# Optimization experiments

Hardware: AMD Instinct MI355X
Metric: run time of the kernel (lower is better)

The kernel has to match this reference:

```python
import jax, jax.numpy as jnp
import numpy as np

HD, NH, DH, NL = 768, 16, 48, 3
EPS = 1e-5


def _ln(x, p):
    g, b = p[0], p[1]
    mu = x.mean(-1, keepdims=True)
    var = ((x - mu) ** 2).mean(-1, keepdims=True)
    return (x - mu) * jax.lax.rsqrt(var + EPS) * g + b


def _init_mlp(x, w1, b1, ln1, w2, b2, ln2):
    h = jax.nn.relu(_ln(x @ w1.T + b1, ln1))
    return jnp.tanh(_ln(h @ w2.T + b2, ln2))


def setup_inputs() -> dict:
    B, S, V = 64, 32, 32000
    key = jax.random.key(0)
    ks = iter(jax.random.split(key, 64))
    rn = lambda shape, s=0.02: jax.random.normal(next(ks), shape, jnp.float32) * s
    lnp = lambda d: jnp.stack([jnp.ones(d, jnp.float32), jnp.zeros(d, jnp.float32)])
    emb = rn((V, 512)).at[0].set(0.0)  # padding_idx=0
    inp = {
        'word_ids': jax.random.randint(next(ks), (B, S), 0, V, jnp.int32),
        'cnn_feat': jax.random.normal(next(ks), (B, HD), jnp.float32),
        'attn_feat': jax.random.normal(next(ks), (B, 2048, 7, 7), jnp.float32),
        'emb': emb,
        'attn_f_w': rn((HD, 2048)), 'attn_f_b': rn((HD,)),
        'attn_qkv_w': rn((3, HD, HD)), 'attn_qkv_b': rn((3, HD)),
        'attn_o_w': rn((HD, HD)), 'attn_o_b': rn((HD,)), 'attn_ln': lnp(HD),
        'fus_w1': rn((HD, 512 + HD)), 'fus_b1': rn((HD,)), 'fus_ln1': lnp(HD),
        'fus_w2': rn((HD, HD)), 'fus_b2': rn((HD,)), 'fus_ln2': lnp(HD),
        'lstm_wih': rn((NL, 4 * HD, HD)), 'lstm_whh': rn((NL, 4 * HD, HD)),
        'lstm_bih': rn((NL, 4 * HD)), 'lstm_bhh': rn((NL, 4 * HD)),
        'hinit_w1': rn((2 * HD, HD)), 'hinit_b1': rn((2 * HD,)), 'hinit_ln1': lnp(2 * HD),
        'hinit_w2': rn((HD, 2 * HD)), 'hinit_b2': rn((HD,)), 'hinit_ln2': lnp(HD),
        'cinit_w1': rn((2 * HD, HD)), 'cinit_b1': rn((2 * HD,)), 'cinit_ln1': lnp(2 * HD),
        'cinit_w2': rn((HD, 2 * HD)), 'cinit_b2': rn((HD,)), 'cinit_ln2': lnp(HD),
        'out_w1': rn((2 * HD, HD)), 'out_b1': rn((2 * HD,)), 'out_ln1': lnp(2 * HD),
        'out_w2': rn((HD, 2 * HD)), 'out_b2': rn((HD,)), 'out_ln2': lnp(HD),
        'out_w3': rn((V, HD)), 'out_b3': rn((V,)),
    }
    return inp


def _forward(word_ids, cnn_feat, attn_feat, emb,
             attn_f_w, attn_f_b, attn_qkv_w, attn_qkv_b, attn_o_w, attn_o_b, attn_ln,
             fus_w1, fus_b1, fus_ln1, fus_w2, fus_b2, fus_ln2,
             lstm_wih, lstm_whh, lstm_bih, lstm_bhh,
             hinit_w1, hinit_b1, hinit_ln1, hinit_w2, hinit_b2, hinit_ln2,
             cinit_w1, cinit_b1, cinit_ln1, cinit_w2, cinit_b2, cinit_ln2,
             out_w1, out_b1, out_ln1, out_w2, out_b2, out_ln2, out_w3, out_b3):
    B, S = word_ids.shape
    # feature projection + K/V are timestep-independent -> hoist out of the loop
    feat = attn_feat.reshape(B, 2048, 49).transpose(0, 2, 1)          # (B,49,2048)
    fp = feat @ attn_f_w.T + attn_f_b                                  # (B,49,HD)
    Wq, Wk, Wv = attn_qkv_w[0], attn_qkv_w[1], attn_qkv_w[2]
    bq, bk, bv = attn_qkv_b[0], attn_qkv_b[1], attn_qkv_b[2]
    K = (fp @ Wk.T + bk).reshape(B, 49, NH, DH).transpose(0, 2, 1, 3)  # (B,NH,49,DH)
    V = (fp @ Wv.T + bv).reshape(B, 49, NH, DH).transpose(0, 2, 1, 3)

    h0 = _init_mlp(cnn_feat, hinit_w1, hinit_b1, hinit_ln1, hinit_w2, hinit_b2, hinit_ln2)
    c0 = _init_mlp(cnn_feat, cinit_w1, cinit_b1, cinit_ln1, cinit_w2, cinit_b2, cinit_ln2)
    h = jnp.tile(h0[None], (NL, 1, 1))                                 # (NL,B,HD)
    c = jnp.tile(c0[None], (NL, 1, 1))

    embeds = emb[word_ids]                                             # (B,S,512)
    scale = np.float32(1.0 / np.sqrt(DH))

    def step(carry, e_t):
        h, c = carry
        q = (h[-1] @ Wq.T + bq).reshape(B, NH, DH)
        scores = jnp.einsum('bhd,bhkd->bhk', q, K) * scale
        w = jax.nn.softmax(scores, axis=-1)
        ctx = jnp.einsum('bhk,bhkd->bhd', w, V).reshape(B, HD)
        ctx = _ln(ctx @ attn_o_w.T + attn_o_b, attn_ln)
        x = jnp.concatenate([e_t, ctx], axis=1)                        # (B,512+HD)
        x = jax.nn.relu(_ln(x @ fus_w1.T + fus_b1, fus_ln1))
        x = jax.nn.relu(_ln(x @ fus_w2.T + fus_b2, fus_ln2))
        inp = x
        hs, cs = [], []
        for l in range(NL):
            g = inp @ lstm_wih[l].T + lstm_bih[l] + h[l] @ lstm_whh[l].T + lstm_bhh[l]
            i, f, gg, o = jnp.split(g, 4, axis=-1)                     # torch gate order
            cn = jax.nn.sigmoid(f) * c[l] + jax.nn.sigmoid(i) * jnp.tanh(gg)
            hn = jax.nn.sigmoid(o) * jnp.tanh(cn)
            hs.append(hn); cs.append(cn); inp = hn
        h = jnp.stack(hs); c = jnp.stack(cs)
        y = jax.nn.relu(_ln(inp @ out_w1.T + out_b1, out_ln1))
        y = jax.nn.relu(_ln(y @ out_w2.T + out_b2, out_ln2))
        logits = y @ out_w3.T + out_b3                                 # (B,V)
        return (h, c), logits

    (hf, cf), ys = jax.lax.scan(step, (h, c), embeds.transpose(1, 0, 2))
    return ys.transpose(1, 0, 2), hf, cf


def reference(word_ids, cnn_feat, attn_feat, emb,
              attn_f_w, attn_f_b, attn_qkv_w, attn_qkv_b, attn_o_w, attn_o_b, attn_ln,
              fus_w1, fus_b1, fus_ln1, fus_w2, fus_b2, fus_ln2,
              lstm_wih, lstm_whh, lstm_bih, lstm_bhh,
              hinit_w1, hinit_b1, hinit_ln1, hinit_w2, hinit_b2, hinit_ln2,
              cinit_w1, cinit_b1, cinit_ln1, cinit_w2, cinit_b2, cinit_ln2,
              out_w1, out_b1, out_ln1, out_w2, out_b2, out_ln2, out_w3, out_b3):
    return _forward(word_ids, cnn_feat, attn_feat, emb,
                    attn_f_w, attn_f_b, attn_qkv_w, attn_qkv_b, attn_o_w, attn_o_b, attn_ln,
                    fus_w1, fus_b1, fus_ln1, fus_w2, fus_b2, fus_ln2,
                    lstm_wih, lstm_whh, lstm_bih, lstm_bhh,
                    hinit_w1, hinit_b1, hinit_ln1, hinit_w2, hinit_b2, hinit_ln2,
                    cinit_w1, cinit_b1, cinit_ln1, cinit_w2, cinit_b2, cinit_ln2,
                    out_w1, out_b1, out_ln1, out_w2, out_b2, out_ln2, out_w3, out_b3)
```

## Files before the change

kernel.cpp:

```cpp
#include <hip/hip_runtime.h>
#include <hip/hip_bf16.h>

enum { B_ = 64, S_ = 32, V_ = 32000, HDIM = 768, NHEAD = 16, DHEAD = 48, NLAY = 3 };
#define LN_EPS 1e-5f

typedef __bf16 bf16_t;
typedef __bf16 bf8 __attribute__((ext_vector_type(8)));
typedef __bf16 bf4v __attribute__((ext_vector_type(4)));
typedef float f4 __attribute__((ext_vector_type(4)));

__device__ __forceinline__ float sigm(float x) { return 1.f / (1.f + expf(-x)); }

__device__ __forceinline__ f4 mfma16x16x32(bf8 a, bf8 b, f4 c) {
    return __builtin_amdgcn_mfma_f32_16x16x32_bf16(a, b, c, 0, 0, 0);
}

__global__ __launch_bounds__(256) void cast_bf16_4(const float4* __restrict__ x,
                                                   bf4v* __restrict__ y, int n4) {
    int i = blockIdx.x * 256 + threadIdx.x;
    int st = gridDim.x * 256;
    for (; i < n4; i += st) {
        float4 v = x[i];
        bf4v o;
        o.x = (__bf16)v.x; o.y = (__bf16)v.y; o.z = (__bf16)v.z; o.w = (__bf16)v.w;
        y[i] = o;
    }
}

template <int OUTBF, int REMAP>
__global__ __launch_bounds__(256) void gemm_mf(const bf16_t* __restrict__ A, int lda,
                                               const bf16_t* __restrict__ W, int ldw,
                                               const float* __restrict__ bias,
                                               void* __restrict__ Cv, int ldc, int K) {
    const int lane = threadIdx.x & 63, wv = threadIdx.x >> 6;
    const int r = lane & 15, kg = lane >> 4;
    const int m0 = blockIdx.y * 64 + wv * 16;
    const int n0 = blockIdx.x * 64;
    const bf16_t* Ar = A + (size_t)(m0 + r) * lda + kg * 8;
    const bf16_t* W0 = W + (size_t)(n0 + r) * ldw + kg * 8;
    f4 acc[4] = {};
#pragma unroll 2
    for (int k0 = 0; k0 < K; k0 += 32) {
        bf8 a = *(const bf8*)(Ar + k0);
#pragma unroll
        for (int j = 0; j < 4; ++j) {
            bf8 b = *(const bf8*)(W0 + (size_t)j * 16 * ldw + k0);
            acc[j] = mfma16x16x32(a, b, acc[j]);
        }
    }
#pragma unroll
    for (int j = 0; j < 4; ++j) {
        int n = n0 + j * 16 + r;
        float bz = bias[n];
#pragma unroll
        for (int i = 0; i < 4; ++i) {
            int m = m0 + kg * 4 + i;
            float v = acc[j][i] + bz;
            if (REMAP) {
                int tt = m >> 6, bb = m & 63;
                ((float*)Cv)[((size_t)bb * S_ + tt) * V_ + n] = v;
            } else if (OUTBF) {
                ((bf16_t*)Cv)[(size_t)m * ldc + n] = (__bf16)v;
            } else {
                ((float*)Cv)[(size_t)m * ldc + n] = v;
            }
        }
    }
}

__global__ __launch_bounds__(256) void gemm_lstm(const bf16_t* __restrict__ X,
                                                 const bf16_t* __restrict__ Wih,
                                                 const bf16_t* __restrict__ H,
                                                 const bf16_t* __restrict__ Whh,
                                                 const float* __restrict__ b1,
                                                 const float* __restrict__ b2,
                                                 float* __restrict__ G) {
    const int lane = threadIdx.x & 63, wv = threadIdx.x >> 6;
    const int r = lane & 15, kg = lane >> 4;
    const int m0 = wv * 16;
    const int n0 = blockIdx.x * 64;
    const bf16_t* Xr = X + (size_t)(m0 + r) * HDIM + kg * 8;
    const bf16_t* Hr = H + (size_t)(m0 + r) * HDIM + kg * 8;
    const bf16_t* Wi = Wih + (size_t)(n0 + r) * HDIM + kg * 8;
    const bf16_t* Wh = Whh + (size_t)(n0 + r) * HDIM + kg * 8;
    f4 acc[4] = {};
#pragma unroll 2
    for (int k0 = 0; k0 < HDIM; k0 += 32) {
        bf8 ax = *(const bf8*)(Xr + k0);
        bf8 ah = *(const bf8*)(Hr + k0);
#pragma unroll
        for (int j = 0; j < 4; ++j) {
            acc[j] = mfma16x16x32(ax, *(const bf8*)(Wi + (size_t)j * 16 * HDIM + k0), acc[j]);
            acc[j] = mfma16x16x32(ah, *(const bf8*)(Wh + (size_t)j * 16 * HDIM + k0), acc[j]);
        }
    }
#pragma unroll
    for (int j = 0; j < 4; ++j) {
        int n = n0 + j * 16 + r;
        float bz = b1[n] + b2[n];
#pragma unroll
        for (int i = 0; i < 4; ++i) {
            int m = m0 + kg * 4 + i;
            G[(size_t)m * (4 * HDIM) + n] = acc[j][i] + bz;
        }
    }
}

__global__ __launch_bounds__(256) void gemm_fus1(const bf16_t* __restrict__ embB,
                                                 const bf16_t* __restrict__ ctxB, int t,
                                                 const bf16_t* __restrict__ W,
                                                 const float* __restrict__ bias,
                                                 float* __restrict__ C) {
    const int lane = threadIdx.x & 63, wv = threadIdx.x >> 6;
    const int r = lane & 15, kg = lane >> 4;
    const int m0 = wv * 16;
    const int n0 = blockIdx.x * 64;
    const int mr = m0 + r;
    const bf16_t* W0 = W + (size_t)(n0 + r) * 1280 + kg * 8;
    const bf16_t* eRow = embB + ((size_t)mr * S_ + t) * 512 + kg * 8;
    const bf16_t* cRow = ctxB + (size_t)mr * HDIM + kg * 8;
    f4 acc[4] = {};
#pragma unroll 2
    for (int k0 = 0; k0 < 1280; k0 += 32) {
        bf8 a = (k0 < 512) ? *(const bf8*)(eRow + k0) : *(const bf8*)(cRow + (k0 - 512));
#pragma unroll
        for (int j = 0; j < 4; ++j) {
            bf8 b = *(const bf8*)(W0 + (size_t)j * 16 * 1280 + k0);
            acc[j] = mfma16x16x32(a, b, acc[j]);
        }
    }
#pragma unroll
    for (int j = 0; j < 4; ++j) {
        int n = n0 + j * 16 + r;
        float bz = bias[n];
#pragma unroll
        for (int i = 0; i < 4; ++i) {
            int m = m0 + kg * 4 + i;
            C[(size_t)m * HDIM + n] = acc[j][i] + bz;
        }
    }
}

__global__ __launch_bounds__(256) void transpose_feat(const float* __restrict__ af,
                                                      bf16_t* __restrict__ feat) {
    __shared__ float t[32][33];
    int b = blockIdx.z;
    int c0 = blockIdx.x * 32;
    int p0 = blockIdx.y * 32;
    int tx = threadIdx.x, ty = threadIdx.y;
    const float* src = af + (size_t)b * 2048 * 49;
    for (int i = ty; i < 32; i += 8) {
        int c = c0 + i, p = p0 + tx;
        t[i][tx] = (p < 49) ? src[(size_t)c * 49 + p] : 0.f;
    }
    __syncthreads();
    bf16_t* dst = feat + (size_t)b * 49 * 2048;
    for (int i = ty; i < 32; i += 8) {
        int p = p0 + i, c = c0 + tx;
        if (p < 49) dst[(size_t)p * 2048 + c] = (__bf16)t[tx][i];
    }
}

__global__ void gather_emb(const int* __restrict__ ids, const float* __restrict__ emb,
                           bf16_t* __restrict__ out) {
    int r = blockIdx.x;
    int w = ids[r];
    const float* e = emb + (size_t)w * 512;
    bf16_t* o = out + (size_t)r * 512;
    for (int i = threadIdx.x; i < 512; i += 256) o[i] = (__bf16)e[i];
}

__global__ __launch_bounds__(256) void ln_act(const float* __restrict__ X,
                                              const float* __restrict__ lnp,
                                              float* __restrict__ Y,
                                              bf16_t* __restrict__ Yb, int N, int act) {
    int r = blockIdx.x;
    const float* x = X + (size_t)r * N;
    float* y = Y + (size_t)r * N;
    bf16_t* yb = Yb ? (Yb + (size_t)r * N) : nullptr;
    float s1 = 0.f, s2 = 0.f;
    for (int i = threadIdx.x; i < N; i += 256) {
        float v = x[i];
        s1 += v;
        s2 += v * v;
    }
#pragma unroll
    for (int off = 32; off > 0; off >>= 1) {
        s1 += __shfl_down(s1, off, 64);
        s2 += __shfl_down(s2, off, 64);
    }
    __shared__ float a1[4], a2[4];
    __shared__ float mu_s, rs_s;
    int lane = threadIdx.x & 63, wid = threadIdx.x >> 6;
    if (lane == 0) { a1[wid] = s1; a2[wid] = s2; }
    __syncthreads();
    if (threadIdx.x == 0) {
        float S1 = a1[0] + a1[1] + a1[2] + a1[3];
        float S2 = a2[0] + a2[1] + a2[2] + a2[3];
        float mu = S1 / N;
        float var = S2 / N - mu * mu;
        mu_s = mu;
        rs_s = rsqrtf(var + LN_EPS);
    }
    __syncthreads();
    float mu = mu_s, rs = rs_s;
    for (int i = threadIdx.x; i < N; i += 256) {
        float v = (x[i] - mu) * rs * lnp[i] + lnp[N + i];
        if (act == 1) v = fmaxf(v, 0.f);
        else if (act == 2) v = tanhf(v);
        y[i] = v;
        if (yb) yb[i] = (__bf16)v;
    }
}

__global__ __launch_bounds__(64) void attn_ctx(const float* __restrict__ q,
                                               const float* __restrict__ Kf,
                                               const float* __restrict__ Vf,
                                               bf16_t* __restrict__ ctx) {
    int b = blockIdx.x, h = blockIdx.y;
    int t = threadIdx.x;
    __shared__ float qs[48];
    __shared__ float w[49];
    if (t < 48) qs[t] = q[(size_t)b * HDIM + h * DHEAD + t];
    __syncthreads();
    if (t < 49) {
        const float* kr = Kf + (size_t)(b * 49 + t) * HDIM + h * DHEAD;
        float s = 0.f;
#pragma unroll
        for (int d = 0; d < 48; ++d) s += qs[d] * kr[d];
        w[t] = s * 0.14433756729740643f;
    }
    __syncthreads();
    if (t == 0) {
        float mx = w[0];
        for (int p = 1; p < 49; ++p) mx = fmaxf(mx, w[p]);
        float sum = 0.f;
        for (int p = 0; p < 49; ++p) {
            float e = expf(w[p] - mx);
            w[p] = e;
            sum += e;
        }
        float inv = 1.f / sum;
        for (int p = 0; p < 49; ++p) w[p] *= inv;
    }
    __syncthreads();
    if (t < 48) {
        float acc = 0.f;
        for (int p = 0; p < 49; ++p) acc += w[p] * Vf[(size_t)(b * 49 + p) * HDIM + h * DHEAD + t];
        ctx[(size_t)b * HDIM + h * DHEAD + t] = (__bf16)acc;
    }
}

__global__ void lstm_cell(const float* __restrict__ g, float* __restrict__ c,
                          float* __restrict__ h, bf16_t* __restrict__ hb,
                          bf16_t* __restrict__ Hcb, int t) {
    int idx = blockIdx.x * 256 + threadIdx.x;
    if (idx >= B_ * HDIM) return;
    int b = idx / HDIM, j = idx - b * HDIM;
    const float* gr = g + (size_t)b * 4 * HDIM;
    float iv = sigm(gr[j]);
    float fv = sigm(gr[HDIM + j]);
    float gv = tanhf(gr[2 * HDIM + j]);
    float ov = sigm(gr[3 * HDIM + j]);
    float cn = fv * c[idx] + iv * gv;
    float hn = ov * tanhf(cn);
    c[idx] = cn;
    h[idx] = hn;
    hb[idx] = (__bf16)hn;
    if (Hcb) Hcb[((size_t)t * B_ + b) * HDIM + j] = (__bf16)hn;
}

__global__ void tile_state(const float* __restrict__ h0, const float* __restrict__ c0,
                           float* __restrict__ h, float* __restrict__ c,
                           bf16_t* __restrict__ hb) {
    int idx = blockIdx.x * 256 + threadIdx.x;
    if (idx >= B_ * HDIM) return;
    float hv = h0[idx], cv = c0[idx];
#pragma unroll
    for (int l = 0; l < NLAY; ++l) {
        h[(size_t)l * B_ * HDIM + idx] = hv;
        c[(size_t)l * B_ * HDIM + idx] = cv;
        hb[(size_t)l * B_ * HDIM + idx] = (__bf16)hv;
    }
}

extern "C" void kernel_launch(void* const* d_in, const int* in_sizes, int n_in,
                              void* d_out, int out_size, void* d_ws, size_t ws_size,
                              hipStream_t stream) {
    const int* word_ids  = (const int*)d_in[0];
    const float* cnn     = (const float*)d_in[1];
    const float* attn_f  = (const float*)d_in[2];
    const float* emb     = (const float*)d_in[3];
    const float* af_w    = (const float*)d_in[4];
    const float* af_b    = (const float*)d_in[5];
    const float* qkv_w   = (const float*)d_in[6];
    const float* qkv_b   = (const float*)d_in[7];
    const float* o_w     = (const float*)d_in[8];
    const float* o_b     = (const float*)d_in[9];
    const float* attn_ln = (const float*)d_in[10];
    const float* fus_w1  = (const float*)d_in[11];
    const float* fus_b1  = (const float*)d_in[12];
    const float* fus_ln1 = (const float*)d_in[13];
    const float* fus_w2  = (const float*)d_in[14];
    const float* fus_b2  = (const float*)d_in[15];
    const float* fus_ln2 = (const float*)d_in[16];
    const float* wih     = (const float*)d_in[17];
    const float* whh     = (const float*)d_in[18];
    const float* bih     = (const float*)d_in[19];
    const float* bhh     = (const float*)d_in[20];
    const float* hi_w1   = (const float*)d_in[21];
    const float* hi_b1   = (const float*)d_in[22];
    const float* hi_ln1  = (const float*)d_in[23];
    const float* hi_w2   = (const float*)d_in[24];
    const float* hi_b2   = (const float*)d_in[25];
    const float* hi_ln2  = (const float*)d_in[26];
    const float* ci_w1   = (const float*)d_in[27];
    const float* ci_b1   = (const float*)d_in[28];
    const float* ci_ln1  = (const float*)d_in[29];
    const float* ci_w2   = (const float*)d_in[30];
    const float* ci_b2   = (const float*)d_in[31];
    const float* ci_ln2  = (const float*)d_in[32];
    const float* out_w1  = (const float*)d_in[33];
    const float* out_b1  = (const float*)d_in[34];
    const float* out_ln1 = (const float*)d_in[35];
    const float* out_w2  = (const float*)d_in[36];
    const float* out_b2  = (const float*)d_in[37];
    const float* out_ln2 = (const float*)d_in[38];
    const float* out_w3  = (const float*)d_in[39];
    const float* out_b3  = (const float*)d_in[40];
    float* outf = (float*)d_out;

    char* wsb = (char*)d_ws;
    size_t off = 0;
    auto allocB = [&](size_t bytes) {
        char* p = wsb + off;
        off += (bytes + 255) & ~(size_t)255;
        return p;
    };
    auto allocF = [&](size_t n) { return (float*)allocB(n * 4); };
    auto allocH = [&](size_t n) { return (bf16_t*)allocB(n * 2); };

    bf16_t* featb  = allocH((size_t)3136 * 2048);
    bf16_t* fpb    = allocH((size_t)3136 * HDIM);
    bf16_t* emb_sb = allocH((size_t)B_ * S_ * 512);
    bf16_t* af_wb  = allocH((size_t)HDIM * 2048);
    bf16_t* qkv_wb = allocH((size_t)3 * HDIM * HDIM);
    bf16_t* o_wb   = allocH((size_t)HDIM * HDIM);
    bf16_t* fus_w1b= allocH((size_t)HDIM * 1280);
    bf16_t* fus_w2b= allocH((size_t)HDIM * HDIM);
    bf16_t* wihb   = allocH((size_t)NLAY * 4 * HDIM * HDIM);
    bf16_t* whhb   = allocH((size_t)NLAY * 4 * HDIM * HDIM);
    bf16_t* hi_w1b = allocH((size_t)1536 * HDIM);
    bf16_t* hi_w2b = allocH((size_t)HDIM * 1536);
    bf16_t* ci_w1b = allocH((size_t)1536 * HDIM);
    bf16_t* ci_w2b = allocH((size_t)HDIM * 1536);
    bf16_t* out_w1b= allocH((size_t)1536 * HDIM);
    bf16_t* out_w2b= allocH((size_t)HDIM * 1536);
    bf16_t* out_w3b= allocH((size_t)V_ * HDIM);
    bf16_t* cnnb   = allocH((size_t)B_ * HDIM);
    bf16_t* hstb   = allocH((size_t)NLAY * B_ * HDIM);
    bf16_t* tmpB   = allocH((size_t)B_ * 1536);
    bf16_t* ctxB   = allocH((size_t)B_ * HDIM);
    bf16_t* ctx2B  = allocH((size_t)B_ * HDIM);
    bf16_t* x1B    = allocH((size_t)B_ * HDIM);
    bf16_t* x2B    = allocH((size_t)B_ * HDIM);
    float* Kf      = allocF((size_t)3136 * HDIM);
    float* Vf      = allocF((size_t)3136 * HDIM);
    float* hst     = allocF((size_t)NLAY * B_ * HDIM);
    float* cst     = allocF((size_t)NLAY * B_ * HDIM);
    float* tmp1536 = allocF((size_t)B_ * 1536);
    float* h0b     = allocF((size_t)B_ * HDIM);
    float* c0b     = allocF((size_t)B_ * HDIM);
    float* qb      = allocF((size_t)B_ * HDIM);
    float* ctx2f   = allocF((size_t)B_ * HDIM);
    float* x1f     = allocF((size_t)B_ * HDIM);
    float* x2f     = allocF((size_t)B_ * HDIM);
    float* gb      = allocF((size_t)B_ * 4 * HDIM);
    float* Y1f     = allocF((size_t)2048 * 1536);
    if (off > ws_size) return;

    bf16_t* HcB = featb;
    bf16_t* Y1B = featb + (size_t)2048 * HDIM;
    bf16_t* Y2B = Y1B + (size_t)2048 * 1536;
    float*  Y2f = Y1f;

    const size_t WQKV = (size_t)HDIM * HDIM;
    const size_t LBH = (size_t)B_ * HDIM;

    auto cast = [&](const float* src, bf16_t* dst, size_t n) {
        int n4 = (int)(n / 4);
        int blocks = (n4 + 255) / 256;
        if (blocks > 1024) blocks = 1024;
        cast_bf16_4<<<blocks, 256, 0, stream>>>((const float4*)src, (bf4v*)dst, n4);
    };

    cast(af_w,   af_wb,   (size_t)HDIM * 2048);
    cast(qkv_w,  qkv_wb,  (size_t)3 * HDIM * HDIM);
    cast(o_w,    o_wb,    (size_t)HDIM * HDIM);
    cast(fus_w1, fus_w1b, (size_t)HDIM * 1280);
    cast(fus_w2, fus_w2b, (size_t)HDIM * HDIM);
    cast(wih,    wihb,    (size_t)NLAY * 4 * HDIM * HDIM);
    cast(whh,    whhb,    (size_t)NLAY * 4 * HDIM * HDIM);
    cast(hi_w1,  hi_w1b,  (size_t)1536 * HDIM);
    cast(hi_w2,  hi_w2b,  (size_t)HDIM * 1536);
    cast(ci_w1,  ci_w1b,  (size_t)1536 * HDIM);
    cast(ci_w2,  ci_w2b,  (size_t)HDIM * 1536);
    cast(out_w1, out_w1b, (size_t)1536 * HDIM);
    cast(out_w2, out_w2b, (size_t)HDIM * 1536);
    cast(out_w3, out_w3b, (size_t)V_ * HDIM);
    cast(cnn,    cnnb,    (size_t)B_ * HDIM);

    gather_emb<<<B_ * S_, 256, 0, stream>>>(word_ids, emb, emb_sb);
    transpose_feat<<<dim3(64, 2, B_), dim3(32, 8), 0, stream>>>(attn_f, featb);
    gemm_mf<1, 0><<<dim3(12, 49), 256, 0, stream>>>(featb, 2048, af_wb, 2048, af_b, fpb, HDIM, 2048);
    gemm_mf<0, 0><<<dim3(12, 49), 256, 0, stream>>>(fpb, HDIM, qkv_wb + WQKV, HDIM, qkv_b + HDIM, Kf, HDIM, HDIM);
    gemm_mf<0, 0><<<dim3(12, 49), 256, 0, stream>>>(fpb, HDIM, qkv_wb + 2 * WQKV, HDIM, qkv_b + 2 * HDIM, Vf, HDIM, HDIM);
    gemm_mf<0, 0><<<dim3(24, 1), 256, 0, stream>>>(cnnb, HDIM, hi_w1b, HDIM, hi_b1, tmp1536, 1536, HDIM);
    ln_act<<<B_, 256, 0, stream>>>(tmp1536, hi_ln1, tmp1536, tmpB, 1536, 1);
    gemm_mf<0, 0><<<dim3(12, 1), 256, 0, stream>>>(tmpB, 1536, hi_w2b, 1536, hi_b2, h0b, HDIM, 1536);
    ln_act<<<B_, 256, 0, stream>>>(h0b, hi_ln2, h0b, nullptr, HDIM, 2);
    gemm_mf<0, 0><<<dim3(24, 1), 256, 0, stream>>>(cnnb, HDIM, ci_w1b, HDIM, ci_b1, tmp1536, 1536, HDIM);
    ln_act<<<B_, 256, 0, stream>>>(tmp1536, ci_ln1, tmp1536, tmpB, 1536, 1);
    gemm_mf<0, 0><<<dim3(12, 1), 256, 0, stream>>>(tmpB, 1536, ci_w2b, 1536, ci_b2, c0b, HDIM, 1536);
    ln_act<<<B_, 256, 0, stream>>>(c0b, ci_ln2, c0b, nullptr, HDIM, 2);
    tile_state<<<192, 256, 0, stream>>>(h0b, c0b, hst, cst, hstb);

    for (int t = 0; t < S_; ++t) {
        gemm_mf<0, 0><<<dim3(12, 1), 256, 0, stream>>>(hstb + 2 * LBH, HDIM, qkv_wb, HDIM, qkv_b, qb, HDIM, HDIM);
        attn_ctx<<<dim3(B_, NHEAD), 64, 0, stream>>>(qb, Kf, Vf, ctxB);
        gemm_mf<0, 0><<<dim3(12, 1), 256, 0, stream>>>(ctxB, HDIM, o_wb, HDIM, o_b, ctx2f, HDIM, HDIM);
        ln_act<<<B_, 256, 0, stream>>>(ctx2f, attn_ln, ctx2f, ctx2B, HDIM, 0);
        gemm_fus1<<<dim3(12, 1), 256, 0, stream>>>(emb_sb, ctx2B, t, fus_w1b, fus_b1, x1f);
        ln_act<<<B_, 256, 0, stream>>>(x1f, fus_ln1, x1f, x1B, HDIM, 1);
        gemm_mf<0, 0><<<dim3(12, 1), 256, 0, stream>>>(x1B, HDIM, fus_w2b, HDIM, fus_b2, x2f, HDIM, HDIM);
        ln_act<<<B_, 256, 0, stream>>>(x2f, fus_ln2, x2f, x2B, HDIM, 1);
        for (int l = 0; l < NLAY; ++l) {
            const bf16_t* inp = (l == 0) ? x2B : (hstb + (size_t)(l - 1) * LBH);
            gemm_lstm<<<dim3(48, 1), 256, 0, stream>>>(inp,
                                                       wihb + (size_t)l * 4 * HDIM * HDIM,
                                                       hstb + (size_t)l * LBH,
                                                       whhb + (size_t)l * 4 * HDIM * HDIM,
                                                       bih + (size_t)l * 4 * HDIM,
                                                       bhh + (size_t)l * 4 * HDIM, gb);
            lstm_cell<<<192, 256, 0, stream>>>(gb, cst + (size_t)l * LBH, hst + (size_t)l * LBH,
                                               hstb + (size_t)l * LBH,
                                               (l == NLAY - 1) ? HcB : nullptr, t);
        }
    }

    gemm_mf<0, 0><<<dim3(24, 32), 256, 0, stream>>>(HcB, HDIM, out_w1b, HDIM, out_b1, Y1f, 1536, HDIM);
    ln_act<<<B_ * S_, 256, 0, stream>>>(Y1f, out_ln1, Y1f, Y1B, 1536, 1);
    gemm_mf<0, 0><<<dim3(12, 32), 256, 0, stream>>>(Y1B, 1536, out_w2b, 1536, out_b2, Y2f, HDIM, 1536);
    ln_act<<<B_ * S_, 256, 0, stream>>>(Y2f, out_ln2, Y2f, Y2B, HDIM, 1);
    gemm_mf<0, 1><<<dim3(500, 32), 256, 0, stream>>>(Y2B, HDIM, out_w3b, HDIM, out_b3, outf, V_, HDIM);

    size_t ys_elems = (size_t)B_ * S_ * V_;
    hipMemcpyAsync(outf + ys_elems, hst, NLAY * LBH * sizeof(float), hipMemcpyDeviceToDevice, stream);
    hipMemcpyAsync(outf + ys_elems + NLAY * LBH, cst, NLAY * LBH * sizeof(float), hipMemcpyDeviceToDevice, stream);
}
```

Before: 8.965 ms.

## Fuse recurrent decode loop into persistent kernel with grid barriers

Replaces the per-timestep chain of about 14 small kernel launches (q projection, attention, o-proj, layernorms, fusion MLP, LSTM GEMM and cell) with one persistent 48-block kernel. The stages are separated by atomic-counter grid barriers. LayerNorm statistics are gathered with atomics in each GEMM epilogue and applied while loading the next GEMM's operands, and the LSTM cell is fused into the gate GEMM using double-buffered hidden states. It also merges the 15 weight-cast launches into a single multi-segment kernel. The aim is to remove launch overhead and intermediate round trips, at the cost of barrier spin latency, low parallelism with only 48 blocks, and the assumption that all blocks are co-resident.

Result: slower. 10.73 ms (+19.7%).

```diff
diff --git a/kernel.cpp b/kernel.cpp
--- a/kernel.cpp
+++ b/kernel.cpp
@@ -3,6 +3,7 @@
 
 enum { B_ = 64, S_ = 32, V_ = 32000, HDIM = 768, NHEAD = 16, DHEAD = 48, NLAY = 3 };
 #define LN_EPS 1e-5f
+#define NBLK 48
 
 typedef __bf16 bf16_t;
 typedef __bf16 bf8 __attribute__((ext_vector_type(8)));
@@ -15,15 +16,25 @@
     return __builtin_amdgcn_mfma_f32_16x16x32_bf16(a, b, c, 0, 0, 0);
 }
 
-__global__ __launch_bounds__(256) void cast_bf16_4(const float4* __restrict__ x,
-                                                   bf4v* __restrict__ y, int n4) {
-    int i = blockIdx.x * 256 + threadIdx.x;
-    int st = gridDim.x * 256;
-    for (; i < n4; i += st) {
-        float4 v = x[i];
-        bf4v o;
-        o.x = (__bf16)v.x; o.y = (__bf16)v.y; o.z = (__bf16)v.z; o.w = (__bf16)v.w;
-        y[i] = o;
+#define NSEG 15
+struct CastSegs {
+    const float4* src[NSEG];
+    bf4v* dst[NSEG];
+    unsigned n4[NSEG];
+};
+__global__ __launch_bounds__(256) void cast_multi(CastSegs cs) {
+    const unsigned stride = gridDim.x * 256;
+#pragma unroll
+    for (int s = 0; s < NSEG; ++s) {
+        const float4* src = cs.src[s];
+        bf4v* dst = cs.dst[s];
+        const unsigned n4 = cs.n4[s];
+        for (unsigned i = blockIdx.x * 256 + threadIdx.x; i < n4; i += stride) {
+            float4 v = src[i];
+            bf4v o;
+            o.x = (__bf16)v.x; o.y = (__bf16)v.y; o.z = (__bf16)v.z; o.w = (__bf16)v.w;
+            dst[i] = o;
+        }
     }
 }
 
@@ -68,79 +79,6 @@
     }
 }
 
-__global__ __launch_bounds__(256) void gemm_lstm(const bf16_t* __restrict__ X,
-                                                 const bf16_t* __restrict__ Wih,
-                                                 const bf16_t* __restrict__ H,
-                                                 const bf16_t* __restrict__ Whh,
-                                                 const float* __restrict__ b1,
-                                                 const float* __restrict__ b2,
-                                                 float* __restrict__ G) {
-    const int lane = threadIdx.x & 63, wv = threadIdx.x >> 6;
-    const int r = lane & 15, kg = lane >> 4;
-    const int m0 = wv * 16;
-    const int n0 = blockIdx.x * 64;
-    const bf16_t* Xr = X + (size_t)(m0 + r) * HDIM + kg * 8;
-    const bf16_t* Hr = H + (size_t)(m0 + r) * HDIM + kg * 8;
-    const bf16_t* Wi = Wih + (size_t)(n0 + r) * HDIM + kg * 8;
-    const bf16_t* Wh = Whh + (size_t)(n0 + r) * HDIM + kg * 8;
-    f4 acc[4] = {};
-#pragma unroll 2
-    for (int k0 = 0; k0 < HDIM; k0 += 32) {
-        bf8 ax = *(const bf8*)(Xr + k0);
-        bf8 ah = *(const bf8*)(Hr + k0);
-#pragma unroll
-        for (int j = 0; j < 4; ++j) {
-            acc[j] = mfma16x16x32(ax, *(const bf8*)(Wi + (size_t)j * 16 * HDIM + k0), acc[j]);
-            acc[j] = mfma16x16x32(ah, *(const bf8*)(Wh + (size_t)j * 16 * HDIM + k0), acc[j]);
-        }
-    }
-#pragma unroll
-    for (int j = 0; j < 4; ++j) {
-        int n = n0 + j * 16 + r;
-        float bz = b1[n] + b2[n];
-#pragma unroll
-        for (int i = 0; i < 4; ++i) {
-            int m = m0 + kg * 4 + i;
-            G[(size_t)m * (4 * HDIM) + n] = acc[j][i] + bz;
-        }
-    }
-}
-
-__global__ __launch_bounds__(256) void gemm_fus1(const bf16_t* __restrict__ embB,
-                                                 const bf16_t* __restrict__ ctxB, int t,
-                                                 const bf16_t* __restrict__ W,
-                                                 const float* __restrict__ bias,
-                                                 float* __restrict__ C) {
-    const int lane = threadIdx.x & 63, wv = threadIdx.x >> 6;
-    const int r = lane & 15, kg = lane >> 4;
-    const int m0 = wv * 16;
-    const int n0 = blockIdx.x * 64;
-    const int mr = m0 + r;
-    const bf16_t* W0 = W + (size_t)(n0 + r) * 1280 + kg * 8;
-    const bf16_t* eRow = embB + ((size_t)mr * S_ + t) * 512 + kg * 8;
-    const bf16_t* cRow = ctxB + (size_t)mr * HDIM + kg * 8;
-    f4 acc[4] = {};
-#pragma unroll 2
-    for (int k0 = 0; k0 < 1280; k0 += 32) {
-        bf8 a = (k0 < 512) ? *(const bf8*)(eRow + k0) : *(const bf8*)(cRow + (k0 - 512));
-#pragma unroll
-        for (int j = 0; j < 4; ++j) {
-            bf8 b = *(const bf8*)(W0 + (size_t)j * 16 * 1280 + k0);
-            acc[j] = mfma16x16x32(a, b, acc[j]);
-        }
-    }
-#pragma unroll
-    for (int j = 0; j < 4; ++j) {
-        int n = n0 + j * 16 + r;
-        float bz = bias[n];
-#pragma unroll
-        for (int i = 0; i < 4; ++i) {
-            int m = m0 + kg * 4 + i;
-            C[(size_t)m * HDIM + n] = acc[j][i] + bz;
-        }
-    }
-}
-
 __global__ __launch_bounds__(256) void transpose_feat(const float* __restrict__ af,
                                                       bf16_t* __restrict__ feat) {
     __shared__ float t[32][33];
@@ -213,63 +151,6 @@
     }
 }
 
-__global__ __launch_bounds__(64) void attn_ctx(const float* __restrict__ q,
-                                               const float* __restrict__ Kf,
-                                               const float* __restrict__ Vf,
-                                               bf16_t* __restrict__ ctx) {
-    int b = blockIdx.x, h = blockIdx.y;
-    int t = threadIdx.x;
-    __shared__ float qs[48];
-    __shared__ float w[49];
-    if (t < 48) qs[t] = q[(size_t)b * HDIM + h * DHEAD + t];
-    __syncthreads();
-    if (t < 49) {
-        const float* kr = Kf + (size_t)(b * 49 + t) * HDIM + h * DHEAD;
-        float s = 0.f;
-#pragma unroll
-        for (int d = 0; d < 48; ++d) s += qs[d] * kr[d];
-        w[t] = s * 0.14433756729740643f;
-    }
-    __syncthreads();
-    if (t == 0) {
-        float mx = w[0];
-        for (int p = 1; p < 49; ++p) mx = fmaxf(mx, w[p]);
-        float sum = 0.f;
-        for (int p = 0; p < 49; ++p) {
-            float e = expf(w[p] - mx);
-            w[p] = e;
-            sum += e;
-        }
-        float inv = 1.f / sum;
-        for (int p = 0; p < 49; ++p) w[p] *= inv;
-    }
-    __syncthreads();
-    if (t < 48) {
-        float acc = 0.f;
-        for (int p = 0; p < 49; ++p) acc += w[p] * Vf[(size_t)(b * 49 + p) * HDIM + h * DHEAD + t];
-        ctx[(size_t)b * HDIM + h * DHEAD + t] = (__bf16)acc;
-    }
-}
-
-__global__ void lstm_cell(const float* __restrict__ g, float* __restrict__ c,
-                          float* __restrict__ h, bf16_t* __restrict__ hb,
-                          bf16_t* __restrict__ Hcb, int t) {
-    int idx = blockIdx.x * 256 + threadIdx.x;
-    if (idx >= B_ * HDIM) return;
-    int b = idx / HDIM, j = idx - b * HDIM;
-    const float* gr = g + (size_t)b * 4 * HDIM;
-    float iv = sigm(gr[j]);
-    float fv = sigm(gr[HDIM + j]);
-    float gv = tanhf(gr[2 * HDIM + j]);
-    float ov = sigm(gr[3 * HDIM + j]);
-    float cn = fv * c[idx] + iv * gv;
-    float hn = ov * tanhf(cn);
-    c[idx] = cn;
-    h[idx] = hn;
-    hb[idx] = (__bf16)hn;
-    if (Hcb) Hcb[((size_t)t * B_ + b) * HDIM + j] = (__bf16)hn;
-}
-
 __global__ void tile_state(const float* __restrict__ h0, const float* __restrict__ c0,
                            float* __restrict__ h, float* __restrict__ c,
                            bf16_t* __restrict__ hb) {
@@ -281,6 +162,263 @@
         h[(size_t)l * B_ * HDIM + idx] = hv;
         c[(size_t)l * B_ * HDIM + idx] = cv;
         hb[(size_t)l * B_ * HDIM + idx] = (__bf16)hv;
+    }
+}
+
+__device__ __forceinline__ void gbar(unsigned* cnt, unsigned* bi) {
+    __syncthreads();
+    if (threadIdx.x == 0) {
+        __threadfence();
+        __hip_atomic_fetch_add(cnt, 1u, __ATOMIC_ACQ_REL, __HIP_MEMORY_SCOPE_AGENT);
+        unsigned target = ++(*bi) * NBLK;
+        while (__hip_atomic_load(cnt, __ATOMIC_ACQUIRE, __HIP_MEMORY_SCOPE_AGENT) < target)
+            __builtin_amdgcn_s_sleep(2);
+        __threadfence();
+    }
+    __syncthreads();
+}
+
+__global__ __launch_bounds__(256) void mega_loop(
+    const bf16_t* __restrict__ qkv_wb, const float* __restrict__ qkv_b,
+    const float* __restrict__ Kf, const float* __restrict__ Vf,
+    const bf16_t* __restrict__ o_wb, const float* __restrict__ o_b,
+    const float* __restrict__ attn_ln,
+    const bf16_t* __restrict__ emb_sb,
+    const bf16_t* __restrict__ fus_w1b, const float* __restrict__ fus_b1,
+    const float* __restrict__ fus_ln1,
+    const bf16_t* __restrict__ fus_w2b, const float* __restrict__ fus_b2,
+    const float* __restrict__ fus_ln2,
+    const bf16_t* __restrict__ wihb, const bf16_t* __restrict__ whhb,
+    const float* __restrict__ bih, const float* __restrict__ bhh,
+    float* __restrict__ hst, float* __restrict__ cst,
+    bf16_t* __restrict__ hbufA, bf16_t* __restrict__ hbufB,
+    float* __restrict__ qb, bf16_t* __restrict__ ctxB, float* __restrict__ ctx2f,
+    float* __restrict__ x1f, float* __restrict__ x2f,
+    float* __restrict__ stats, bf16_t* __restrict__ HcB,
+    unsigned* __restrict__ cnt) {
+    const int tid = threadIdx.x;
+    const int lane = tid & 63, wv = tid >> 6;
+    const int blk = blockIdx.x;
+    const int r = lane & 15, kg = lane >> 4;
+    const int m0 = wv * 16;
+    const int n0 = blk * 16;
+    const size_t LBH = (size_t)B_ * HDIM;
+    unsigned bi = 0;
+    bf16_t* cur = hbufA;
+    bf16_t* nxt = hbufB;
+
+    for (int t = 0; t < S_; ++t) {
+        {
+            const bf16_t* Ar = cur + 2 * LBH + (size_t)(m0 + r) * HDIM + kg * 8;
+            const bf16_t* Wr = qkv_wb + (size_t)(n0 + r) * HDIM + kg * 8;
+            f4 acc = {};
+#pragma unroll 4
+            for (int k0 = 0; k0 < HDIM; k0 += 32)
+                acc = mfma16x16x32(*(const bf8*)(Ar + k0), *(const bf8*)(Wr + k0), acc);
+            const int n = n0 + r;
+            const float bz = qkv_b[n];
+#pragma unroll
+            for (int i = 0; i < 4; ++i)
+                qb[(size_t)(m0 + kg * 4 + i) * HDIM + n] = acc[i] + bz;
+        }
+        gbar(cnt, &bi);
+        {
+            for (int p = blk * 4 + wv; p < B_ * NHEAD; p += NBLK * 4) {
+                const int b = p >> 4, h = p & 15;
+                const float* qrow = qb + (size_t)b * HDIM + h * DHEAD;
+                float s = -1e30f;
+                if (lane < 49) {
+                    const float* kr = Kf + (size_t)(b * 49 + lane) * HDIM + h * DHEAD;
+                    float a = 0.f;
+#pragma unroll
+                    for (int d = 0; d < DHEAD; ++d) a += qrow[d] * kr[d];
+                    s = a * 0.14433756729740643f;
+                }
+                float mx = s;
+#pragma unroll
+                for (int o = 32; o; o >>= 1) mx = fmaxf(mx, __shfl_xor(mx, o, 64));
+                const float e = (lane < 49) ? expf(s - mx) : 0.f;
+                float sum = e;
+#pragma unroll
+                for (int o = 32; o; o >>= 1) sum += __shfl_xor(sum, o, 64);
+                const float wgt = e / sum;
+                float a2 = 0.f;
+                const float* vb = Vf + (size_t)(b * 49) * HDIM + h * DHEAD + lane;
+                for (int pp = 0; pp < 49; ++pp) {
+                    const float wp = __shfl(wgt, pp, 64);
+                    if (lane < DHEAD) a2 += wp * vb[(size_t)pp * HDIM];
+                }
+                if (lane < DHEAD) ctxB[(size_t)b * HDIM + h * DHEAD + lane] = (__bf16)a2;
+            }
+        }
+        gbar(cnt, &bi);
+        {
+            const bf16_t* Ar = ctxB + (size_t)(m0 + r) * HDIM + kg * 8;
+            const bf16_t* Wr = o_wb + (size_t)(n0 + r) * HDIM + kg * 8;
+            f4 acc = {};
+#pragma unroll 4
+            for (int k0 = 0; k0 < HDIM; k0 += 32)
+                acc = mfma16x16x32(*(const bf8*)(Ar + k0), *(const bf8*)(Wr + k0), acc);
+            const int n = n0 + r;
+            const float bz = o_b[n];
+            float* st = stats + ((size_t)t * 3 + 0) * 128;
+#pragma unroll
+            for (int i = 0; i < 4; ++i) {
+                const int row = m0 + kg * 4 + i;
+                const float v = acc[i] + bz;
+                ctx2f[(size_t)row * HDIM + n] = v;
+                float p1 = v, p2 = v * v;
+#pragma unroll
+                for (int m = 1; m < 16; m <<= 1) {
+                    p1 += __shfl_xor(p1, m, 64);
+                    p2 += __shfl_xor(p2, m, 64);
+                }
+                if (r == 0) { atomicAdd(&st[row], p1); atomicAdd(&st[64 + row], p2); }
+            }
+        }
+        gbar(cnt, &bi);
+        {
+            const int arow = m0 + r;
+            const float* st0 = stats + ((size_t)t * 3 + 0) * 128;
+            const float mu = st0[arow] * (1.f / HDIM);
+            const float rs = rsqrtf(st0[64 + arow] * (1.f / HDIM) - mu * mu + LN_EPS);
+            const float la = rs, lc = -mu * rs;
+            const bf16_t* eRow = emb_sb + ((size_t)arow * S_ + t) * 512 + kg * 8;
+            const float* xRow = ctx2f + (size_t)arow * HDIM + kg * 8;
+            const bf16_t* Wr = fus_w1b + (size_t)(n0 + r) * 1280 + kg * 8;
+            f4 acc = {};
+#pragma unroll 4
+            for (int k0 = 0; k0 < 1280; k0 += 32) {
+                bf8 a;
+                if (k0 < 512) {
+                    a = *(const bf8*)(eRow + k0);
+                } else {
+                    const int kk = k0 - 512;
+#pragma unroll
+                    for (int j = 0; j < 8; ++j) {
+                        const int kj = kk + kg * 8 + j;
+                        a[j] = (__bf16)((xRow[kk + j] * la + lc) * attn_ln[kj] + attn_ln[HDIM + kj]);
+                    }
+                }
+                acc = mfma16x16x32(a, *(const bf8*)(Wr + k0), acc);
+            }
+            const int n = n0 + r;
+            const float bz = fus_b1[n];
+            float* st = stats + ((size_t)t * 3 + 1) * 128;
+#pragma unroll
+            for (int i = 0; i < 4; ++i) {
+                const int row = m0 + kg * 4 + i;
+                const float v = acc[i] + bz;
+                x1f[(size_t)row * HDIM + n] = v;
+                float p1 = v, p2 = v * v;
+#pragma unroll
+                for (int m = 1; m < 16; m <<= 1) {
+                    p1 += __shfl_xor(p1, m, 64);
+                    p2 += __shfl_xor(p2, m, 64);
+                }
+                if (r == 0) { atomicAdd(&st[row], p1); atomicAdd(&st[64 + row], p2); }
+            }
+        }
+        gbar(cnt, &bi);
+        {
+            const int arow = m0 + r;
+            const float* st1 = stats + ((size_t)t * 3 + 1) * 128;
+            const float mu = st1[arow] * (1.f / HDIM);
+            const float rs = rsqrtf(st1[64 + arow] * (1.f / HDIM) - mu * mu + LN_EPS);
+            const float la = rs, lc = -mu * rs;
+            const float* xRow = x1f + (size_t)arow * HDIM + kg * 8;
+            const bf16_t* Wr = fus_w2b + (size_t)(n0 + r) * HDIM + kg * 8;
+            f4 acc = {};
+#pragma unroll 4
+            for (int k0 = 0; k0 < HDIM; k0 += 32) {
+                bf8 a;
+#pragma unroll
+                for (int j = 0; j < 8; ++j) {
+                    const int kj = k0 + kg * 8 + j;
+                    a[j] = (__bf16)fmaxf((xRow[k0 + j] * la + lc) * fus_ln1[kj] + fus_ln1[HDIM + kj], 0.f);
+                }
+                acc = mfma16x16x32(a, *(const bf8*)(Wr + k0), acc);
+            }
+            const int n = n0 + r;
+            const float bz = fus_b2[n];
+            float* st = stats + ((size_t)t * 3 + 2) * 128;
+#pragma unroll
+            for (int i = 0; i < 4; ++i) {
+                const int row = m0 + kg * 4 + i;
+                const float v = acc[i] + bz;
+                x2f[(size_t)row * HDIM + n] = v;
+                float p1 = v, p2 = v * v;
+#pragma unroll
+                for (int m = 1; m < 16; m <<= 1) {
+                    p1 += __shfl_xor(p1, m, 64);
+                    p2 += __shfl_xor(p2, m, 64);
+                }
+                if (r == 0) { atomicAdd(&st[row], p1); atomicAdd(&st[64 + row], p2); }
+            }
+        }
+        gbar(cnt, &bi);
+        for (int l = 0; l < NLAY; ++l) {
+            const int arow = m0 + r;
+            float la = 0.f, lc = 0.f;
+            if (l == 0) {
+                const float* st2 = stats + ((size_t)t * 3 + 2) * 128;
+                const float mu = st2[arow] * (1.f / HDIM);
+                const float rs = rsqrtf(st2[64 + arow] * (1.f / HDIM) - mu * mu + LN_EPS);
+                la = rs;
+                lc = -mu * rs;
+            }
+            const float* xRow = x2f + (size_t)arow * HDIM + kg * 8;
+            const int lprev = (l == 0) ? 0 : (l - 1);
+            const bf16_t* h1Row = nxt + (size_t)lprev * LBH + (size_t)arow * HDIM + kg * 8;
+            const bf16_t* h2Row = cur + (size_t)l * LBH + (size_t)arow * HDIM + kg * 8;
+            const bf16_t* WiB = wihb + (size_t)l * 4 * HDIM * HDIM + (size_t)(n0 + r) * HDIM + kg * 8;
+            const bf16_t* WhB = whhb + (size_t)l * 4 * HDIM * HDIM + (size_t)(n0 + r) * HDIM + kg * 8;
+            f4 acc0 = {}, acc1 = {}, acc2 = {}, acc3 = {};
+#pragma unroll 2
+            for (int k0 = 0; k0 < HDIM; k0 += 32) {
+                bf8 a1;
+                if (l == 0) {
+#pragma unroll
+                    for (int j = 0; j < 8; ++j) {
+                        const int kj = k0 + kg * 8 + j;
+                        a1[j] = (__bf16)fmaxf((xRow[k0 + j] * la + lc) * fus_ln2[kj] + fus_ln2[HDIM + kj], 0.f);
+                    }
+                } else {
+                    a1 = *(const bf8*)(h1Row + k0);
+                }
+                const bf8 a2 = *(const bf8*)(h2Row + k0);
+                acc0 = mfma16x16x32(a1, *(const bf8*)(WiB + (size_t)0 * HDIM * HDIM + k0), acc0);
+                acc0 = mfma16x16x32(a2, *(const bf8*)(WhB + (size_t)0 * HDIM * HDIM + k0), acc0);
+                acc1 = mfma16x16x32(a1, *(const bf8*)(WiB + (size_t)768 * HDIM + k0), acc1);
+                acc1 = mfma16x16x32(a2, *(const bf8*)(WhB + (size_t)768 * HDIM + k0), acc1);
+                acc2 = mfma16x16x32(a1, *(const bf8*)(WiB + (size_t)1536 * HDIM + k0), acc2);
+                acc2 = mfma16x16x32(a2, *(const bf8*)(WhB + (size_t)1536 * HDIM + k0), acc2);
+                acc3 = mfma16x16x32(a1, *(const bf8*)(WiB + (size_t)2304 * HDIM + k0), acc3);
+                acc3 = mfma16x16x32(a2, *(const bf8*)(WhB + (size_t)2304 * HDIM + k0), acc3);
+            }
+            const int j = n0 + r;
+            const float b0 = bih[l * 3072 + j] + bhh[l * 3072 + j];
+            const float b1 = bih[l * 3072 + 768 + j] + bhh[l * 3072 + 768 + j];
+            const float b2 = bih[l * 3072 + 1536 + j] + bhh[l * 3072 + 1536 + j];
+            const float b3 = bih[l * 3072 + 2304 + j] + bhh[l * 3072 + 2304 + j];
+#pragma unroll
+            for (int i = 0; i < 4; ++i) {
+                const int row = m0 + kg * 4 + i;
+                const float iv = sigm(acc0[i] + b0);
+                const float fv = sigm(acc1[i] + b1);
+                const float gv = tanhf(acc2[i] + b2);
+                const float ov = sigm(acc3[i] + b3);
+                const size_t idx = (size_t)l * LBH + (size_t)row * HDIM + j;
+                const float cn = fv * cst[idx] + iv * gv;
+                const float hn = ov * tanhf(cn);
+                cst[idx] = cn;
+                hst[idx] = hn;
+                nxt[idx] = (__bf16)hn;
+                if (l == NLAY - 1) HcB[((size_t)t * B_ + row) * HDIM + j] = (__bf16)hn;
+            }
+            gbar(cnt, &bi);
+        }
+        bf16_t* tmp = cur; cur = nxt; nxt = tmp;
     }
 }
 
@@ -340,6 +478,9 @@
     auto allocF = [&](size_t n) { return (float*)allocB(n * 4); };
     auto allocH = [&](size_t n) { return (bf16_t*)allocB(n * 2); };
 
+    unsigned* barcnt = (unsigned*)allocB(256);
+    float* stats     = allocF((size_t)S_ * 3 * 128);
+
     bf16_t* featb  = allocH((size_t)3136 * 2048);
     bf16_t* fpb    = allocH((size_t)3136 * HDIM);
     bf16_t* emb_sb = allocH((size_t)B_ * S_ * 512);
@@ -358,12 +499,10 @@
     bf16_t* out_w2b= allocH((size_t)HDIM * 1536);
     bf16_t* out_w3b= allocH((size_t)V_ * HDIM);
     bf16_t* cnnb   = allocH((size_t)B_ * HDIM);
-    bf16_t* hstb   = allocH((size_t)NLAY * B_ * HDIM);
+    bf16_t* hbufA  = allocH((size_t)NLAY * B_ * HDIM);
+    bf16_t* hbufB  = allocH((size_t)NLAY * B_ * HDIM);
     bf16_t* tmpB   = allocH((size_t)B_ * 1536);
     bf16_t* ctxB   = allocH((size_t)B_ * HDIM);
-    bf16_t* ctx2B  = allocH((size_t)B_ * HDIM);
-    bf16_t* x1B    = allocH((size_t)B_ * HDIM);
-    bf16_t* x2B    = allocH((size_t)B_ * HDIM);
     float* Kf      = allocF((size_t)3136 * HDIM);
     float* Vf      = allocF((size_t)3136 * HDIM);
     float* hst     = allocF((size_t)NLAY * B_ * HDIM);
@@ -375,7 +514,6 @@
     float* ctx2f   = allocF((size_t)B_ * HDIM);
     float* x1f     = allocF((size_t)B_ * HDIM);
     float* x2f     = allocF((size_t)B_ * HDIM);
-    float* gb      = allocF((size_t)B_ * 4 * HDIM);
     float* Y1f     = allocF((size_t)2048 * 1536);
     if (off > ws_size) return;
 
@@ -387,28 +525,27 @@
     const size_t WQKV = (size_t)HDIM * HDIM;
     const size_t LBH = (size_t)B_ * HDIM;
 
-    auto cast = [&](const float* src, bf16_t* dst, size_t n) {
-        int n4 = (int)(n / 4);
-        int blocks = (n4 + 255) / 256;
-        if (blocks > 1024) blocks = 1024;
-        cast_bf16_4<<<blocks, 256, 0, stream>>>((const float4*)src, (bf4v*)dst, n4);
-    };
-
-    cast(af_w,   af_wb,   (size_t)HDIM * 2048);
-    cast(qkv_w,  qkv_wb,  (size_t)3 * HDIM * HDIM);
-    cast(o_w,    o_wb,    (size_t)HDIM * HDIM);
-    cast(fus_w1, fus_w1b, (size_t)HDIM * 1280);
-    cast(fus_w2, fus_w2b, (size_t)HDIM * HDIM);
-    cast(wih,    wihb,    (size_t)NLAY * 4 * HDIM * HDIM);
-    cast(whh,    whhb,    (size_t)NLAY * 4 * HDIM * HDIM);
-    cast(hi_w1,  hi_w1b,  (size_t)1536 * HDIM);
-    cast(hi_w2,  hi_w2b,  (size_t)HDIM * 1536);
-    cast(ci_w1,  ci_w1b,  (size_t)1536 * HDIM);
-    cast(ci_w2,  ci_w2b,  (size_t)HDIM * 1536);
-    cast(out_w1, out_w1b, (size_t)1536 * HDIM);
-    cast(out_w2, out_w2b, (size_t)HDIM * 1536);
-    cast(out_w3, out_w3b, (size_t)V_ * HDIM);
-    cast(cnn,    cnnb,    (size_t)B_ * HDIM);
+    hipMemsetAsync(barcnt, 0, 256 + (size_t)S_ * 3 * 128 * 4, stream);
+
+    {
+        CastSegs cs;
+        const float* srcs[NSEG] = {af_w, qkv_w, o_w, fus_w1, fus_w2, wih, whh,
+                                   hi_w1, hi_w2, ci_w1, ci_w2, out_w1, out_w2, out_w3, cnn};
+        bf16_t* dsts[NSEG] = {af_wb, qkv_wb, o_wb, fus_w1b, fus_w2b, wihb, whhb,
+                              hi_w1b, hi_w2b, ci_w1b, ci_w2b, out_w1b, out_w2b, out_w3b, cnnb};
+        const size_t ns[NSEG] = {(size_t)HDIM * 2048, 3 * WQKV, WQKV, (size_t)HDIM * 1280, WQKV,
+                                 (size_t)NLAY * 4 * WQKV, (size_t)NLAY * 4 * WQKV,
+                                 (size_t)1536 * HDIM, (size_t)HDIM * 1536,
+                                 (size_t)1536 * HDIM, (size_t)HDIM * 1536,
+                                 (size_t)1536 * HDIM, (size_t)HDIM * 1536,
+                                 (size_t)V_ * HDIM, (size_t)B_ * HDIM};
+        for (int s = 0; s < NSEG; ++s) {
+            cs.src[s] = (const float4*)srcs[s];
+            cs.dst[s] = (bf4v*)dsts[s];
+            cs.n4[s] = (unsigned)(ns[s] / 4);
+        }
+        cast_multi<<<2048, 256, 0, stream>>>(cs);
+    }
 
     gather_emb<<<B_ * S_, 256, 0, stream>>>(word_ids, emb, emb_sb);
     transpose_feat<<<dim3(64, 2, B_), dim3(32, 8), 0, stream>>>(attn_f, featb);
@@ -423,30 +560,14 @@
     ln_act<<<B_, 256, 0, stream>>>(tmp1536, ci_ln1, tmp1536, tmpB, 1536, 1);
     gemm_mf<0, 0><<<dim3(12, 1), 256, 0, stream>>>(tmpB, 1536, ci_w2b, 1536, ci_b2, c0b, HDIM, 1536);
     ln_act<<<B_, 256, 0, stream>>>(c0b, ci_ln2, c0b, nullptr, HDIM, 2);
-    tile_state<<<192, 256, 0, stream>>>(h0b, c0b, hst, cst, hstb);
-
-    for (int t = 0; t < S_; ++t) {
-        gemm_mf<0, 0><<<dim3(12, 1), 256, 0, stream>>>(hstb + 2 * LBH, HDIM, qkv_wb, HDIM, qkv_b, qb, HDIM, HDIM);
-        attn_ctx<<<dim3(B_, NHEAD), 64, 0, stream>>>(qb, Kf, Vf, ctxB);
-        gemm_mf<0, 0><<<dim3(12, 1), 256, 0, stream>>>(ctxB, HDIM, o_wb, HDIM, o_b, ctx2f, HDIM, HDIM);
-        ln_act<<<B_, 256, 0, stream>>>(ctx2f, attn_ln, ctx2f, ctx2B, HDIM, 0);
-        gemm_fus1<<<dim3(12, 1), 256, 0, stream>>>(emb_sb, ctx2B, t, fus_w1b, fus_b1, x1f);
-        ln_act<<<B_, 256, 0, stream>>>(x1f, fus_ln1, x1f, x1B, HDIM, 1);
-        gemm_mf<0, 0><<<dim3(12, 1), 256, 0, stream>>>(x1B, HDIM, fus_w2b, HDIM, fus_b2, x2f, HDIM, HDIM);
-        ln_act<<<B_, 256, 0, stream>>>(x2f, fus_ln2, x2f, x2B, HDIM, 1);
-        for (int l = 0; l < NLAY; ++l) {
-            const bf16_t* inp = (l == 0) ? x2B : (hstb + (size_t)(l - 1) * LBH);
-            gemm_lstm<<<dim3(48, 1), 256, 0, stream>>>(inp,
-                                                       wihb + (size_t)l * 4 * HDIM * HDIM,
-                                                       hstb + (size_t)l * LBH,
-                                                       whhb + (size_t)l * 4 * HDIM * HDIM,
-                                                       bih + (size_t)l * 4 * HDIM,
-                                                       bhh + (size_t)l * 4 * HDIM, gb);
-            lstm_cell<<<192, 256, 0, stream>>>(gb, cst + (size_t)l * LBH, hst + (size_t)l * LBH,
-                                               hstb + (size_t)l * LBH,
-                                               (l == NLAY - 1) ? HcB : nullptr, t);
-        }
-    }
+    tile_state<<<192, 256, 0, stream>>>(h0b, c0b, hst, cst, hbufA);
+
+    mega_loop<<<NBLK, 256, 0, stream>>>(
+        qkv_wb, qkv_b, Kf, Vf, o_wb, o_b, attn_ln, emb_sb,
+        fus_w1b, fus_b1, fus_ln1, fus_w2b, fus_b2, fus_ln2,
+        wihb, whhb, bih, bhh,
+        hst, cst, hbufA, hbufB, qb, ctxB, ctx2f, x1f, x2f,
+        stats, HcB, barcnt);
 
     gemm_mf<0, 0><<<dim3(24, 32), 256, 0, stream>>>(HcB, HDIM, out_w1b, HDIM, out_b1, Y1f, 1536, HDIM);
     ln_act<<<B_ * S_, 256, 0, stream>>>(Y1f, out_ln1, Y1f, Y1B, 1536, 1);
```
